# Kernel optimization log

Measured on AMD Instinct MI355X. Metric: run time of the kernel, lower is better.

Reference implementation:

```python
import jax, jax.numpy as jnp
import numpy as np

EPS = 1e-5

def layernorm(x, w, b):
    m = jnp.mean(x, axis=-1, keepdims=True)
    v = jnp.var(x, axis=-1, keepdims=True)
    return (x - m) * jax.lax.rsqrt(v + EPS) * w + b

def setup_inputs() -> dict:
    key = jax.random.key(0)
    ks = jax.random.split(key, 20)
    B, N, D, H, C = 4, 2048, 512, 8, 3
    HID = int(D * 4.0 * (2.0 / 3.0))  # SwiGLU hidden = 1365
    g = lambda k, shape, s: (jax.random.normal(k, shape, jnp.float32) * s)
    return {
        "x": g(ks[0], (B, N, D), 1.0),
        "coords": jax.random.uniform(ks[1], (B, N, C), jnp.float32),
        "ln1_w": jnp.ones((D,), jnp.float32),
        "ln1_b": jnp.zeros((D,), jnp.float32),
        "ln2_w": jnp.ones((D,), jnp.float32),
        "ln2_b": jnp.zeros((D,), jnp.float32),
        "Wqkv": g(ks[2], (D, 3 * D), D ** -0.5),
        "bqkv": jnp.zeros((3 * D,), jnp.float32),
        "Wo": g(ks[3], (D, D), D ** -0.5),
        "bo": jnp.zeros((D,), jnp.float32),
        "Wc": g(ks[4], (C, H), 0.1),
        "bc": jnp.zeros((H,), jnp.float32),
        "W1": g(ks[5], (D, HID), D ** -0.5),
        "b1": jnp.zeros((HID,), jnp.float32),
        "W2": g(ks[6], (D, HID), D ** -0.5),
        "b2": jnp.zeros((HID,), jnp.float32),
        "W3": g(ks[7], (HID, D), HID ** -0.5),
        "b3": jnp.zeros((D,), jnp.float32),
    }

def reference(x, coords, ln1_w, ln1_b, ln2_w, ln2_b, Wqkv, bqkv, Wo, bo,
              Wc, bc, W1, b1, W2, b2, W3, b3):
    B, N, D = x.shape
    H = bc.shape[0]
    dh = D // H
    # --- coord-aware patch attention (pre-norm) ---
    h = layernorm(x, ln1_w, ln1_b)
    qkv = h @ Wqkv + bqkv                                # [B,N,3D]
    q, k, v = jnp.split(qkv, 3, axis=-1)
    to_heads = lambda t: t.reshape(B, N, H, dh).transpose(0, 2, 1, 3)  # [B,H,N,dh]
    q, k, v = to_heads(q), to_heads(k), to_heads(v)
    scores = jnp.einsum("bhnd,bhmd->bhnm", q, k) / np.sqrt(dh)
    rel = coords[:, :, None, :] - coords[:, None, :, :]  # [B,N,N,C]
    bias = jnp.einsum("bnmc,ch->bhnm", rel, Wc) + bc[None, :, None, None]
    attn = jax.nn.softmax(scores + bias, axis=-1)
    o = jnp.einsum("bhnm,bhmd->bhnd", attn, v)
    o = o.transpose(0, 2, 1, 3).reshape(B, N, D)
    x = x + (o @ Wo + bo)                                # residual 1
    # --- SwiGLU FFN (pre-norm) ---
    h2 = layernorm(x, ln2_w, ln2_b)
    ff = jax.nn.silu(h2 @ W1 + b1) * (h2 @ W2 + b2)
    x = x + (ff @ W3 + b3)                               # residual 2
    return x
```

## Files before the change

kernel.cpp:

```cpp
#include <hip/hip_runtime.h>
#include <hip/hip_bf16.h>
#include <math.h>

#define B_   4
#define N_   2048
#define D_   512
#define H_   8
#define DH_  64
#define C_   3
#define HID_ 1365
#define HIDP 1408
#define ROWS_ (B_*N_)
#define TD_  (3*D_)

typedef __attribute__((ext_vector_type(8))) short short8;
typedef __attribute__((ext_vector_type(4))) float floatx4;

#define MFMA16(a,b,c) __builtin_amdgcn_mfma_f32_16x16x32_bf16(a,b,c,0,0,0)

typedef __attribute__((address_space(3))) unsigned lds_u32;
typedef __attribute__((address_space(1))) unsigned glb_u32;

__device__ __forceinline__ short sh(float v){
  union { __hip_bfloat16 b; short s; } u;
  u.b = __float2bfloat16(v);
  return u.s;
}

__device__ __forceinline__ int swz(int col, int row){
  return (col & ~63) | (col & 7) | ((((col >> 3) & 7) ^ (row & 7)) << 3);
}

template<int ROWS, int PITCH>
__device__ __forceinline__ void stageG(short* __restrict__ lds,
    const short* __restrict__ g, int ldg, int t){
  const int LPR = PITCH/8;
  const int RPI = 64/LPR;
  const int PW  = (ROWS/RPI)/4;
  int lane = t & 63, w = t >> 6;
  #pragma unroll
  for (int i = 0; i < PW; ++i){
    int r0  = (w*PW + i)*RPI;
    int row = r0 + lane/LPR;
    const short* ga = g + (size_t)row*ldg + (lane % LPR)*8;
    short* la = lds + r0*PITCH;
    __builtin_amdgcn_global_load_lds((const glb_u32*)ga, (lds_u32*)la, 16, 0, 0);
  }
}

__device__ __forceinline__ short8 fragS(const short* __restrict__ lds, int pitch,
    int mbase, int lane, int kk){
  int row  = mbase + (lane & 15);
  int seg  = (kk >> 3) + (lane >> 4);
  int phys = seg ^ (row & 7);
  return *(const short8*)(lds + row*pitch + phys*8);
}

__device__ __forceinline__ short8 fragP(const short* __restrict__ lds,
    int mbase, int lane, int kk){
  return *(const short8*)(lds + (mbase + (lane & 15))*136 + kk + ((lane >> 4) << 3));
}

__global__ __launch_bounds__(256) void convT_all(
    const float* __restrict__ Wqkv, const float* __restrict__ Wo,
    const float* __restrict__ W1, const float* __restrict__ W2,
    const float* __restrict__ W3,
    short* __restrict__ Wtqkv, short* __restrict__ Wto,
    short* __restrict__ Wt1, short* __restrict__ Wt2, short* __restrict__ Wt3,
    const float* __restrict__ coords, const float* __restrict__ Wc,
    float* __restrict__ tv){
  __shared__ float tile[32][33];
  int id = blockIdx.x;
  int t = threadIdx.x;
  if (id >= 3136){
    int idx = (id - 3136)*256 + t;
    int n = idx & (N_-1);
    int hh = (idx >> 11) & (H_-1);
    int b = idx >> 14;
    float s = 0.f;
    #pragma unroll
    for (int cc = 0; cc < C_; ++cc)
      s += coords[((size_t)(b*N_+n))*C_ + cc] * Wc[cc*H_ + hh];
    tv[idx] = s;
    return;
  }
  const float* in; short* out; int K, NN, Kp, nx;
  if (id < 768)      { in=Wqkv; out=Wtqkv; K=512;  NN=1536; Kp=512;  nx=48; }
  else if (id < 1024){ in=Wo;   out=Wto;   K=512;  NN=512;  Kp=512;  nx=16; id-=768; }
  else if (id < 1728){ in=W1;   out=Wt1;   K=512;  NN=HID_; Kp=512;  nx=44; id-=1024; }
  else if (id < 2432){ in=W2;   out=Wt2;   K=512;  NN=HID_; Kp=512;  nx=44; id-=1728; }
  else               { in=W3;   out=Wt3;   K=HID_; NN=512;  Kp=HIDP; nx=16; id-=2432; }
  int nt0 = (id % nx)*32, kt0 = (id / nx)*32;
  int r = t >> 5, cc = t & 31;
  #pragma unroll
  for (int i=0;i<4;++i){
    int k = kt0 + i*8 + r, n = nt0 + cc;
    tile[i*8+r][cc] = (k<K && n<NN) ? in[(size_t)k*NN + n] : 0.f;
  }
  __syncthreads();
  #pragma unroll
  for (int i=0;i<4;++i){
    int n = nt0 + i*8 + r, k = kt0 + cc;
    out[(size_t)n*Kp + swz(k, n)] = sh(tile[cc][i*8+r]);
  }
}

__global__ __launch_bounds__(256) void ln_kernel(const float* __restrict__ x,
        const float* __restrict__ w, const float* __restrict__ b,
        short* __restrict__ out){
  int row = blockIdx.x;
  size_t base = (size_t)row * D_;
  int t = threadIdx.x;
  float v0 = x[base + t];
  float v1 = x[base + t + 256];
  float s  = v0 + v1;
  float s2 = v0*v0 + v1*v1;
  #pragma unroll
  for (int off = 32; off >= 1; off >>= 1){
    s  += __shfl_xor(s,  off, 64);
    s2 += __shfl_xor(s2, off, 64);
  }
  __shared__ float red[8];
  int lane = t & 63, wv = t >> 6;
  if (lane == 0){ red[wv] = s; red[4+wv] = s2; }
  __syncthreads();
  float sum  = red[0]+red[1]+red[2]+red[3];
  float sum2 = red[4]+red[5]+red[6]+red[7];
  float mean = sum * (1.0f/D_);
  float var  = sum2 * (1.0f/D_) - mean*mean;
  float inv  = rsqrtf(fmaxf(var, 0.f) + 1e-5f);
  out[base + swz(t,     row)] = sh((v0-mean)*inv*w[t]     + b[t]);
  out[base + swz(t+256, row)] = sh((v1-mean)*inv*w[t+256] + b[t+256]);
}

__global__ __launch_bounds__(256) void qkv_gemm(
    const short* __restrict__ A, const short* __restrict__ Bt,
    const float* __restrict__ bias,
    short* __restrict__ qb, short* __restrict__ kb, short* __restrict__ vbt){
  __shared__ short As[128*64];
  __shared__ short Bs[128*64];
  int t = threadIdx.x;
  int lane = t & 63, w = t >> 6;
  int wr = (w >> 1) * 64, wc = (w & 1) * 64;
  int col0 = blockIdx.x * 128, row0 = blockIdx.y * 128;
  floatx4 acc[4][4];
  #pragma unroll
  for (int mt=0;mt<4;++mt)
    #pragma unroll
    for (int nt=0;nt<4;++nt) acc[mt][nt] = (floatx4){0.f,0.f,0.f,0.f};
  for (int k0 = 0; k0 < D_; k0 += 64){
    __syncthreads();
    stageG<128,64>(As, A  + (size_t)row0*D_ + k0, D_, t);
    stageG<128,64>(Bs, Bt + (size_t)col0*D_ + k0, D_, t);
    __syncthreads();
    #pragma unroll
    for (int kk = 0; kk < 64; kk += 32){
      short8 af[4], bf[4];
      #pragma unroll
      for (int mt=0;mt<4;++mt) af[mt] = fragS(As, 64, wr+mt*16, lane, kk);
      #pragma unroll
      for (int nt=0;nt<4;++nt) bf[nt] = fragS(Bs, 64, wc+nt*16, lane, kk);
      #pragma unroll
      for (int mt=0;mt<4;++mt)
        #pragma unroll
        for (int nt=0;nt<4;++nt)
          acc[mt][nt] = MFMA16(af[mt], bf[nt], acc[mt][nt]);
    }
  }
  int quad = lane >> 4, c = lane & 15;
  #pragma unroll
  for (int mt=0;mt<4;++mt){
    #pragma unroll
    for (int nt=0;nt<4;++nt){
      #pragma unroll
      for (int r=0;r<4;++r){
        int row = row0 + wr + mt*16 + quad*4 + r;
        int col = col0 + wc + nt*16 + c;
        float v = acc[mt][nt][r] + bias[col];
        int bidx = row >> 11, n = row & (N_-1);
        int which = col >> 9, d = col & (D_-1), hh = d >> 6, hd = d & 63;
        short sv = sh(v);
        if (which == 0)
          qb[(((size_t)(bidx*H_ + hh))*N_ + n)*DH_ + swz(hd, n)] = sv;
        else if (which == 1)
          kb[(((size_t)(bidx*H_ + hh))*N_ + n)*DH_ + swz(hd, n)] = sv;
        else
          vbt[(((size_t)(bidx*H_ + hh))*DH_ + hd)*N_ + swz(n, hd)] = sv;
      }
    }
  }
}

__global__ __launch_bounds__(256) void gemm64(
    const short* __restrict__ A, int lda,
    const short* __restrict__ Bt, int Ktot,
    const float* __restrict__ bias,
    const float* __restrict__ resid, float* __restrict__ outF){
  __shared__ short As[128*64];
  __shared__ short Bs[64*64];
  int t = threadIdx.x, lane = t & 63, w = t >> 6;
  int wr = w * 32;
  int col0 = blockIdx.x * 64, row0 = blockIdx.y * 128;
  floatx4 acc[2][4];
  #pragma unroll
  for (int mt=0;mt<2;++mt)
    #pragma unroll
    for (int nt=0;nt<4;++nt) acc[mt][nt] = (floatx4){0.f,0.f,0.f,0.f};
  for (int k0 = 0; k0 < Ktot; k0 += 64){
    __syncthreads();
    stageG<128,64>(As, A  + (size_t)row0*lda + k0, lda, t);
    stageG<64,64> (Bs, Bt + (size_t)col0*Ktot + k0, Ktot, t);
    __syncthreads();
    #pragma unroll
    for (int kk = 0; kk < 64; kk += 32){
      short8 af[2], bf[4];
      #pragma unroll
      for (int mt=0;mt<2;++mt) af[mt] = fragS(As, 64, wr+mt*16, lane, kk);
      #pragma unroll
      for (int nt=0;nt<4;++nt) bf[nt] = fragS(Bs, 64, nt*16, lane, kk);
      #pragma unroll
      for (int mt=0;mt<2;++mt)
        #pragma unroll
        for (int nt=0;nt<4;++nt)
          acc[mt][nt] = MFMA16(af[mt], bf[nt], acc[mt][nt]);
    }
  }
  int quad = lane >> 4, c = lane & 15;
  #pragma unroll
  for (int mt=0;mt<2;++mt){
    #pragma unroll
    for (int nt=0;nt<4;++nt){
      #pragma unroll
      for (int r=0;r<4;++r){
        int row = row0 + wr + mt*16 + quad*4 + r;
        int col = col0 + nt*16 + c;
        size_t idx = (size_t)row*D_ + col;
        outF[idx] = acc[mt][nt][r] + bias[col] + resid[idx];
      }
    }
  }
}

__global__ __launch_bounds__(256) void gate_gemm(
    const short* __restrict__ A,
    const short* __restrict__ Bt1, const short* __restrict__ Bt2,
    const float* __restrict__ b1, const float* __restrict__ b2,
    short* __restrict__ ff){
  __shared__ short As[128*64];
  __shared__ short B1s[64*64];
  __shared__ short B2s[64*64];
  int t = threadIdx.x, lane = t & 63, w = t >> 6;
  int wr = (w >> 1) * 64, wc = (w & 1) * 32;
  int col0 = blockIdx.x * 64, row0 = blockIdx.y * 128;
  floatx4 a1[4][2], a2[4][2];
  #pragma unroll
  for (int mt=0;mt<4;++mt)
    #pragma unroll
    for (int nt=0;nt<2;++nt){
      a1[mt][nt] = (floatx4){0.f,0.f,0.f,0.f};
      a2[mt][nt] = (floatx4){0.f,0.f,0.f,0.f};
    }
  for (int k0 = 0; k0 < D_; k0 += 64){
    __syncthreads();
    stageG<128,64>(As, A + (size_t)row0*D_ + k0, D_, t);
    stageG<64,64>(B1s, Bt1 + (size_t)col0*D_ + k0, D_, t);
    stageG<64,64>(B2s, Bt2 + (size_t)col0*D_ + k0, D_, t);
    __syncthreads();
    #pragma unroll
    for (int kk = 0; kk < 64; kk += 32){
      short8 af[4], f1[2], f2[2];
      #pragma unroll
      for (int mt=0;mt<4;++mt) af[mt] = fragS(As, 64, wr+mt*16, lane, kk);
      #pragma unroll
      for (int nt=0;nt<2;++nt){
        f1[nt] = fragS(B1s, 64, wc+nt*16, lane, kk);
        f2[nt] = fragS(B2s, 64, wc+nt*16, lane, kk);
      }
      #pragma unroll
      for (int mt=0;mt<4;++mt)
        #pragma unroll
        for (int nt=0;nt<2;++nt){
          a1[mt][nt] = MFMA16(af[mt], f1[nt], a1[mt][nt]);
          a2[mt][nt] = MFMA16(af[mt], f2[nt], a2[mt][nt]);
        }
    }
  }
  int quad = lane >> 4, c = lane & 15;
  #pragma unroll
  for (int mt=0;mt<4;++mt){
    #pragma unroll
    for (int nt=0;nt<2;++nt){
      #pragma unroll
      for (int r=0;r<4;++r){
        int row = row0 + wr + mt*16 + quad*4 + r;
        int col = col0 + wc + nt*16 + c;
        float g1 = a1[mt][nt][r] + (col < HID_ ? b1[col] : 0.f);
        float g2 = a2[mt][nt][r] + (col < HID_ ? b2[col] : 0.f);
        float sig = 1.f / (1.f + __expf(-g1));
        ff[(size_t)row*HIDP + swz(col, row)] = sh(g1*sig*g2);
      }
    }
  }
}

__global__ __launch_bounds__(256) void attn_mfma(
    const short* __restrict__ qb, const short* __restrict__ kb,
    const short* __restrict__ vbt, const float* __restrict__ tv,
    short* __restrict__ o){
  __shared__ short Ks[128*64];
  __shared__ short Vt[64*128];
  __shared__ short Ps[128*136];
  __shared__ float tsh[128];
  int qt = blockIdx.x, h = blockIdx.y, b = blockIdx.z;
  int bh = b*H_ + h;
  int t = threadIdx.x, lane = t & 63, w = t >> 6;
  int quad = lane >> 4, c = lane & 15;
  stageG<128,64>(Ps, qb + ((size_t)bh*N_ + qt*128)*DH_, DH_, t);
  __syncthreads();
  short8 qf[2][2];
  #pragma unroll
  for (int mt=0;mt<2;++mt)
    #pragma unroll
    for (int kh=0;kh<2;++kh)
      qf[mt][kh] = fragS(Ps, 64, w*32 + mt*16, lane, kh*32);

  floatx4 O[2][4];
  float l_i[2][4];
  #pragma unroll
  for (int mt=0;mt<2;++mt){
    #pragma unroll
    for (int nt=0;nt<4;++nt) O[mt][nt] = (floatx4){0.f,0.f,0.f,0.f};
    #pragma unroll
    for (int r=0;r<4;++r) l_i[mt][r] = 0.f;
  }
  const short* Kbase = kb  + (size_t)bh*N_*DH_;
  const short* Vbase = vbt + (size_t)bh*DH_*N_;

  for (int kt = 0; kt < N_/128; ++kt){
    __syncthreads();
    stageG<128,64>(Ks, Kbase + (size_t)kt*128*DH_, DH_, t);
    stageG<64,128>(Vt, Vbase + kt*128, N_, t);
    if (t < 128) tsh[t] = tv[(size_t)bh*N_ + kt*128 + t];
    __syncthreads();

    floatx4 S[2][8];
    #pragma unroll
    for (int mt=0;mt<2;++mt)
      #pragma unroll
      for (int nt=0;nt<8;++nt) S[mt][nt] = (floatx4){0.f,0.f,0.f,0.f};
    #pragma unroll
    for (int kh=0;kh<2;++kh){
      short8 kf[8];
      #pragma unroll
      for (int nt=0;nt<8;++nt) kf[nt] = fragS(Ks, 64, nt*16, lane, kh*32);
      #pragma unroll
      for (int mt=0;mt<2;++mt)
        #pragma unroll
        for (int nt=0;nt<8;++nt)
          S[mt][nt] = MFMA16(qf[mt][kh], kf[nt], S[mt][nt]);
    }
    float ts[8];
    #pragma unroll
    for (int nt=0;nt<8;++nt) ts[nt] = tsh[nt*16 + c];
    #pragma unroll
    for (int mt=0;mt<2;++mt)
      #pragma unroll
      for (int r=0;r<4;++r){
        #pragma unroll
        for (int nt=0;nt<8;++nt){
          float p = __expf(S[mt][nt][r]*0.125f - ts[nt]);
          l_i[mt][r] += p;
          Ps[(w*32 + mt*16 + quad*4 + r)*136 + nt*16 + c] = sh(p);
        }
      }
    asm volatile("s_waitcnt lgkmcnt(0)" ::: "memory");
    #pragma unroll
    for (int kh=0;kh<4;++kh){
      short8 vf[4], pf[2];
      #pragma unroll
      for (int nt=0;nt<4;++nt) vf[nt] = fragS(Vt, 128, nt*16, lane, kh*32);
      #pragma unroll
      for (int mt=0;mt<2;++mt) pf[mt] = fragP(Ps, w*32 + mt*16, lane, kh*32);
      #pragma unroll
      for (int mt=0;mt<2;++mt)
        #pragma unroll
        for (int nt=0;nt<4;++nt)
          O[mt][nt] = MFMA16(pf[mt], vf[nt], O[mt][nt]);
    }
  }
  #pragma unroll
  for (int mt=0;mt<2;++mt){
    #pragma unroll
    for (int r=0;r<4;++r){
      float l = l_i[mt][r];
      #pragma unroll
      for (int off=1; off<16; off<<=1) l += __shfl_xor(l, off, 64);
      float invl = 1.f / l;
      int row = qt*128 + w*32 + mt*16 + quad*4 + r;
      #pragma unroll
      for (int nt=0;nt<4;++nt){
        int col = h*DH_ + nt*16 + c;
        o[((size_t)(b*N_ + row))*D_ + swz(col, row)] = sh(O[mt][nt][r]*invl);
      }
    }
  }
}

extern "C" void kernel_launch(void* const* d_in, const int* in_sizes, int n_in,
                              void* d_out, int out_size, void* d_ws, size_t ws_size,
                              hipStream_t stream){
  const float* x      = (const float*)d_in[0];
  const float* coords = (const float*)d_in[1];
  const float* ln1_w  = (const float*)d_in[2];
  const float* ln1_b  = (const float*)d_in[3];
  const float* ln2_w  = (const float*)d_in[4];
  const float* ln2_b  = (const float*)d_in[5];
  const float* Wqkv   = (const float*)d_in[6];
  const float* bqkv   = (const float*)d_in[7];
  const float* Wo     = (const float*)d_in[8];
  const float* bo     = (const float*)d_in[9];
  const float* Wc     = (const float*)d_in[10];
  const float* W1     = (const float*)d_in[12];
  const float* b1     = (const float*)d_in[13];
  const float* W2     = (const float*)d_in[14];
  const float* b2     = (const float*)d_in[15];
  const float* W3     = (const float*)d_in[16];
  const float* b3     = (const float*)d_in[17];

  char* ws = (char*)d_ws;
  short* Wtqkv = (short*)(ws);
  short* Wto   = (short*)(ws + 1572864);
  short* Wt1   = (short*)(ws + 2097152);
  short* Wt2   = (short*)(ws + 3538944);
  short* Wt3   = (short*)(ws + 4980736);
  float* tv    = (float*)(ws + 6422528);
  short* h     = (short*)(ws + 6684672);
  short* qb    = (short*)(ws + 15073280);
  short* kb    = (short*)(ws + 23461888);
  short* vbt   = (short*)(ws + 31850496);
  short* o     = h;
  short* h2    = h;
  short* ff    = qb;
  float* x1    = (float*)d_out;

  convT_all<<<dim3(3392), dim3(256), 0, stream>>>(Wqkv, Wo, W1, W2, W3,
      Wtqkv, Wto, Wt1, Wt2, Wt3, coords, Wc, tv);
  ln_kernel<<<dim3(ROWS_), dim3(256), 0, stream>>>(x, ln1_w, ln1_b, h);
  qkv_gemm<<<dim3(12,64), dim3(256), 0, stream>>>(h, Wtqkv, bqkv, qb, kb, vbt);
  attn_mfma<<<dim3(16,8,4), dim3(256), 0, stream>>>(qb, kb, vbt, tv, o);
  gemm64<<<dim3(8,64), dim3(256), 0, stream>>>(o, 512, Wto, 512, bo, x, x1);
  ln_kernel<<<dim3(ROWS_), dim3(256), 0, stream>>>(x1, ln2_w, ln2_b, h2);
  gate_gemm<<<dim3(22,64), dim3(256), 0, stream>>>(h2, Wt1, Wt2, b1, b2, ff);
  gemm64<<<dim3(8,64), dim3(256), 0, stream>>>(ff, HIDP, Wt3, HIDP, b3, x1, x1);
}
```

Measured before the change: 317.5 us.

## Fuse first layernorm into prep kernel, widen gate GEMM tile, swizzle P and use exp2

Merges the first layernorm into the weight-conversion launch as extra blocks, removing one kernel launch. Doubles the gate GEMM column tile to 128 so each A tile is reused across more output columns. Swaps the padded P buffer in attention for an XOR-swizzled layout and folds log2(e) into the coordinate bias and scale so exp2 can be used. The larger gate tile raises register and LDS use, which may lower occupancy; the layernorm now uses a single-pass E[x^2]-mean^2 variance.

```diff
diff --git a/kernel.cpp b/kernel.cpp
--- a/kernel.cpp
+++ b/kernel.cpp
@@ -56,11 +56,6 @@
   return *(const short8*)(lds + row*pitch + phys*8);
 }
 
-__device__ __forceinline__ short8 fragP(const short* __restrict__ lds,
-    int mbase, int lane, int kk){
-  return *(const short8*)(lds + (mbase + (lane & 15))*136 + kk + ((lane >> 4) << 3));
-}
-
 __global__ __launch_bounds__(256) void convT_all(
     const float* __restrict__ Wqkv, const float* __restrict__ Wo,
     const float* __restrict__ W1, const float* __restrict__ W2,
@@ -68,10 +63,36 @@
     short* __restrict__ Wtqkv, short* __restrict__ Wto,
     short* __restrict__ Wt1, short* __restrict__ Wt2, short* __restrict__ Wt3,
     const float* __restrict__ coords, const float* __restrict__ Wc,
-    float* __restrict__ tv){
-  __shared__ float tile[32][33];
+    float* __restrict__ tu,
+    const float* __restrict__ x, const float* __restrict__ ln1_w,
+    const float* __restrict__ ln1_b, short* __restrict__ h){
   int id = blockIdx.x;
   int t = threadIdx.x;
+  if (id >= 3392){
+    int row = id - 3392;
+    size_t base = (size_t)row * D_;
+    float v0 = x[base + t];
+    float v1 = x[base + t + 256];
+    float s  = v0 + v1;
+    float s2 = v0*v0 + v1*v1;
+    #pragma unroll
+    for (int off = 32; off >= 1; off >>= 1){
+      s  += __shfl_xor(s,  off, 64);
+      s2 += __shfl_xor(s2, off, 64);
+    }
+    __shared__ float red[8];
+    int lane = t & 63, wv = t >> 6;
+    if (lane == 0){ red[wv] = s; red[4+wv] = s2; }
+    __syncthreads();
+    float sum  = red[0]+red[1]+red[2]+red[3];
+    float sum2 = red[4]+red[5]+red[6]+red[7];
+    float mean = sum * (1.0f/D_);
+    float var  = sum2 * (1.0f/D_) - mean*mean;
+    float inv  = rsqrtf(fmaxf(var, 0.f) + 1e-5f);
+    h[base + swz(t,     row)] = sh((v0-mean)*inv*ln1_w[t]     + ln1_b[t]);
+    h[base + swz(t+256, row)] = sh((v1-mean)*inv*ln1_w[t+256] + ln1_b[t+256]);
+    return;
+  }
   if (id >= 3136){
     int idx = (id - 3136)*256 + t;
     int n = idx & (N_-1);
@@ -81,9 +102,10 @@
     #pragma unroll
     for (int cc = 0; cc < C_; ++cc)
       s += coords[((size_t)(b*N_+n))*C_ + cc] * Wc[cc*H_ + hh];
-    tv[idx] = s;
+    tu[idx] = s * 1.44269504f;
     return;
   }
+  __shared__ float tile[32][33];
   const float* in; short* out; int K, NN, Kp, nx;
   if (id < 768)      { in=Wqkv; out=Wtqkv; K=512;  NN=1536; Kp=512;  nx=48; }
   else if (id < 1024){ in=Wo;   out=Wto;   K=512;  NN=512;  Kp=512;  nx=16; id-=768; }
@@ -247,39 +269,39 @@
     const float* __restrict__ b1, const float* __restrict__ b2,
     short* __restrict__ ff){
   __shared__ short As[128*64];
-  __shared__ short B1s[64*64];
-  __shared__ short B2s[64*64];
+  __shared__ short B1s[128*64];
+  __shared__ short B2s[128*64];
   int t = threadIdx.x, lane = t & 63, w = t >> 6;
-  int wr = (w >> 1) * 64, wc = (w & 1) * 32;
-  int col0 = blockIdx.x * 64, row0 = blockIdx.y * 128;
-  floatx4 a1[4][2], a2[4][2];
+  int wr = (w >> 1) * 64, wc = (w & 1) * 64;
+  int col0 = blockIdx.x * 128, row0 = blockIdx.y * 128;
+  floatx4 a1[4][4], a2[4][4];
   #pragma unroll
   for (int mt=0;mt<4;++mt)
     #pragma unroll
-    for (int nt=0;nt<2;++nt){
+    for (int nt=0;nt<4;++nt){
       a1[mt][nt] = (floatx4){0.f,0.f,0.f,0.f};
       a2[mt][nt] = (floatx4){0.f,0.f,0.f,0.f};
     }
   for (int k0 = 0; k0 < D_; k0 += 64){
     __syncthreads();
-    stageG<128,64>(As, A + (size_t)row0*D_ + k0, D_, t);
-    stageG<64,64>(B1s, Bt1 + (size_t)col0*D_ + k0, D_, t);
-    stageG<64,64>(B2s, Bt2 + (size_t)col0*D_ + k0, D_, t);
+    stageG<128,64>(As,  A   + (size_t)row0*D_ + k0, D_, t);
+    stageG<128,64>(B1s, Bt1 + (size_t)col0*D_ + k0, D_, t);
+    stageG<128,64>(B2s, Bt2 + (size_t)col0*D_ + k0, D_, t);
     __syncthreads();
     #pragma unroll
     for (int kk = 0; kk < 64; kk += 32){
-      short8 af[4], f1[2], f2[2];
+      short8 af[4], f1[4], f2[4];
       #pragma unroll
       for (int mt=0;mt<4;++mt) af[mt] = fragS(As, 64, wr+mt*16, lane, kk);
       #pragma unroll
-      for (int nt=0;nt<2;++nt){
+      for (int nt=0;nt<4;++nt){
         f1[nt] = fragS(B1s, 64, wc+nt*16, lane, kk);
         f2[nt] = fragS(B2s, 64, wc+nt*16, lane, kk);
       }
       #pragma unroll
       for (int mt=0;mt<4;++mt)
         #pragma unroll
-        for (int nt=0;nt<2;++nt){
+        for (int nt=0;nt<4;++nt){
           a1[mt][nt] = MFMA16(af[mt], f1[nt], a1[mt][nt]);
           a2[mt][nt] = MFMA16(af[mt], f2[nt], a2[mt][nt]);
         }
@@ -289,7 +311,7 @@
   #pragma unroll
   for (int mt=0;mt<4;++mt){
     #pragma unroll
-    for (int nt=0;nt<2;++nt){
+    for (int nt=0;nt<4;++nt){
       #pragma unroll
       for (int r=0;r<4;++r){
         int row = row0 + wr + mt*16 + quad*4 + r;
@@ -305,12 +327,12 @@
 
 __global__ __launch_bounds__(256) void attn_mfma(
     const short* __restrict__ qb, const short* __restrict__ kb,
-    const short* __restrict__ vbt, const float* __restrict__ tv,
+    const short* __restrict__ vbt, const float* __restrict__ tu,
     short* __restrict__ o){
   __shared__ short Ks[128*64];
   __shared__ short Vt[64*128];
-  __shared__ short Ps[128*136];
-  __shared__ float tsh[128];
+  __shared__ short Ps[128*128];
+  __shared__ float ush[128];
   int qt = blockIdx.x, h = blockIdx.y, b = blockIdx.z;
   int bh = b*H_ + h;
   int t = threadIdx.x, lane = t & 63, w = t >> 6;
@@ -340,7 +362,7 @@
     __syncthreads();
     stageG<128,64>(Ks, Kbase + (size_t)kt*128*DH_, DH_, t);
     stageG<64,128>(Vt, Vbase + kt*128, N_, t);
-    if (t < 128) tsh[t] = tv[(size_t)bh*N_ + kt*128 + t];
+    if (t < 128) ush[t] = tu[(size_t)bh*N_ + kt*128 + t];
     __syncthreads();
 
     floatx4 S[2][8];
@@ -359,18 +381,19 @@
         for (int nt=0;nt<8;++nt)
           S[mt][nt] = MFMA16(qf[mt][kh], kf[nt], S[mt][nt]);
     }
-    float ts[8];
-    #pragma unroll
-    for (int nt=0;nt<8;++nt) ts[nt] = tsh[nt*16 + c];
+    float u8[8];
+    #pragma unroll
+    for (int nt=0;nt<8;++nt) u8[nt] = ush[nt*16 + c];
     #pragma unroll
     for (int mt=0;mt<2;++mt)
       #pragma unroll
       for (int r=0;r<4;++r){
+        int prow = w*32 + mt*16 + quad*4 + r;
         #pragma unroll
         for (int nt=0;nt<8;++nt){
-          float p = __expf(S[mt][nt][r]*0.125f - ts[nt]);
+          float p = exp2f(fmaf(S[mt][nt][r], 0.18033688f, -u8[nt]));
           l_i[mt][r] += p;
-          Ps[(w*32 + mt*16 + quad*4 + r)*136 + nt*16 + c] = sh(p);
+          Ps[prow*128 + swz(nt*16 + c, prow)] = sh(p);
         }
       }
     asm volatile("s_waitcnt lgkmcnt(0)" ::: "memory");
@@ -380,7 +403,7 @@
       #pragma unroll
       for (int nt=0;nt<4;++nt) vf[nt] = fragS(Vt, 128, nt*16, lane, kh*32);
       #pragma unroll
-      for (int mt=0;mt<2;++mt) pf[mt] = fragP(Ps, w*32 + mt*16, lane, kh*32);
+      for (int mt=0;mt<2;++mt) pf[mt] = fragS(Ps, 128, w*32 + mt*16, lane, kh*32);
       #pragma unroll
       for (int mt=0;mt<2;++mt)
         #pragma unroll
@@ -433,7 +456,7 @@
   short* Wt1   = (short*)(ws + 2097152);
   short* Wt2   = (short*)(ws + 3538944);
   short* Wt3   = (short*)(ws + 4980736);
-  float* tv    = (float*)(ws + 6422528);
+  float* tu    = (float*)(ws + 6422528);
   short* h     = (short*)(ws + 6684672);
   short* qb    = (short*)(ws + 15073280);
   short* kb    = (short*)(ws + 23461888);
@@ -443,13 +466,12 @@
   short* ff    = qb;
   float* x1    = (float*)d_out;
 
-  convT_all<<<dim3(3392), dim3(256), 0, stream>>>(Wqkv, Wo, W1, W2, W3,
-      Wtqkv, Wto, Wt1, Wt2, Wt3, coords, Wc, tv);
-  ln_kernel<<<dim3(ROWS_), dim3(256), 0, stream>>>(x, ln1_w, ln1_b, h);
+  convT_all<<<dim3(11584), dim3(256), 0, stream>>>(Wqkv, Wo, W1, W2, W3,
+      Wtqkv, Wto, Wt1, Wt2, Wt3, coords, Wc, tu, x, ln1_w, ln1_b, h);
   qkv_gemm<<<dim3(12,64), dim3(256), 0, stream>>>(h, Wtqkv, bqkv, qb, kb, vbt);
-  attn_mfma<<<dim3(16,8,4), dim3(256), 0, stream>>>(qb, kb, vbt, tv, o);
+  attn_mfma<<<dim3(16,8,4), dim3(256), 0, stream>>>(qb, kb, vbt, tu, o);
   gemm64<<<dim3(8,64), dim3(256), 0, stream>>>(o, 512, Wto, 512, bo, x, x1);
   ln_kernel<<<dim3(ROWS_), dim3(256), 0, stream>>>(x1, ln2_w, ln2_b, h2);
-  gate_gemm<<<dim3(22,64), dim3(256), 0, stream>>>(h2, Wt1, Wt2, b1, b2, ff);
+  gate_gemm<<<dim3(11,64), dim3(256), 0, stream>>>(h2, Wt1, Wt2, b1, b2, ff);
   gemm64<<<dim3(8,64), dim3(256), 0, stream>>>(ff, HIDP, Wt3, HIDP, b3, x1, x1);
 }
```

Result: slower. 395.6 us (+24.6%).
